# Optimization experiments

Hardware: AMD Instinct MI355X
Metric: run time of the kernel (lower is better)

## Reference

```python
import jax, jax.numpy as jnp
import numpy as np

B, SEQ, K, H = 4096, 50, 4, 64   # batch, seq_len, interest_num, hidden_size
ROUTING_TIMES = 3


def setup_inputs() -> dict:
    key = jax.random.key(0)
    k1, k2, k3 = jax.random.split(key, 3)
    mask = jax.random.randint(k1, (B, SEQ), 0, 2, dtype=jnp.int32)
    item_eb_hat = jax.random.normal(k2, (B, SEQ, K, H), dtype=jnp.float32)
    capsule_weight = jax.random.normal(k3, (B, K, SEQ), dtype=jnp.float32)
    return {"mask": mask, "item_eb_hat": item_eb_hat, "capsule_weight": capsule_weight}


def _squash(v):
    # v: [B, K, 1, H]
    cap_norm = jnp.sum(jnp.square(v), -1, keepdims=True)
    scalar = cap_norm / (1.0 + cap_norm) / jnp.sqrt(cap_norm + 1e-9)
    return scalar * v


def reference(mask, item_eb_hat, capsule_weight):
    # [B, seq, K, H] -> [B, K, seq, H]
    x = jnp.transpose(item_eb_hat.reshape(-1, SEQ, K, H), (0, 2, 1, 3))
    x_iter = jax.lax.stop_gradient(x)  # stop_grad=True in the module
    # attention mask broadcast to [B, K, seq]
    am = jnp.broadcast_to(mask[:, None, :], capsule_weight.shape)
    interest_capsule = None
    for i in range(ROUTING_TIMES):
        # torch F.softmax without dim on a 3D tensor -> dim=0 (batch axis); faithful.
        w = jax.nn.softmax(capsule_weight, axis=0)
        w = jnp.where(am == 0, jnp.zeros_like(w), w)[:, :, None, :]  # [B,K,1,seq]
        if i < ROUTING_TIMES - 1:
            interest_capsule = _squash(jnp.matmul(w, x_iter))          # [B,K,1,H]
            delta = jnp.matmul(x_iter, jnp.swapaxes(interest_capsule, -1, -2))  # [B,K,seq,1]
            capsule_weight = capsule_weight + delta.reshape(-1, K, SEQ)
        else:
            interest_capsule = _squash(jnp.matmul(w, x))               # [B,K,1,H]
    return interest_capsule.reshape(-1, K, H)
```

## Files before the change

### kernel.cpp

```cpp
#include <hip/hip_runtime.h>
#include <math.h>

#define BB 4096
#define SEQ 50
#define KK 4
#define HH 64
#define NCOL (KK*SEQ)

__global__ void colstats_kernel(const float* __restrict__ cw,
                                float* __restrict__ colmax,
                                float* __restrict__ colsum) {
    const int col = blockIdx.x;
    const int t = threadIdx.x;

    float m = -INFINITY, l = 0.f;
#pragma unroll
    for (int i = 0; i < BB / 256; i++) {
        float v = cw[(size_t)(i * 256 + t) * NCOL + col];
        float nm = fmaxf(m, v);
        l = l * __expf(m - nm) + __expf(v - nm);
        m = nm;
    }
#pragma unroll
    for (int off = 32; off >= 1; off >>= 1) {
        float om = __shfl_xor(m, off, 64);
        float ol = __shfl_xor(l, off, 64);
        float nm = fmaxf(m, om);
        l = l * __expf(m - nm) + ol * __expf(om - nm);
        m = nm;
    }
    __shared__ float sm[4], sl[4];
    const int wid = t >> 6;
    if ((t & 63) == 0) { sm[wid] = m; sl[wid] = l; }
    __syncthreads();
    if (t == 0) {
        m = sm[0]; l = sl[0];
#pragma unroll
        for (int w = 1; w < 4; w++) {
            float om = sm[w], ol = sl[w];
            float nm = fmaxf(m, om);
            l = l * __expf(m - nm) + ol * __expf(om - nm);
            m = nm;
        }
        colmax[col] = m;
        colsum[col] = l;
    }
}

template <bool FINAL>
__global__ void update_kernel(const float* __restrict__ cw_src,
                              float* __restrict__ cw_dst,
                              const float* __restrict__ x,
                              const int* __restrict__ mask,
                              const float* __restrict__ colmax,
                              const float* __restrict__ colsum,
                              float* __restrict__ out) {
    const int b = blockIdx.x;
    const int k = threadIdx.x >> 6;
    const int h = threadIdx.x & 63;

    const float* xp = x + (size_t)b * (SEQ * KK * HH) + k * HH + h;
    float xrow[SEQ];
#pragma unroll
    for (int s = 0; s < SEQ; s++) xrow[s] = xp[s * (KK * HH)];

    float wlane = 0.f, c = 0.f;
    if (h < SEQ) {
        const int col = k * SEQ + h;
        c = cw_src[(size_t)b * NCOL + col];
        float e = __expf(c - colmax[col]) / colsum[col];
        wlane = (mask[b * SEQ + h] != 0) ? e : 0.f;
    }

    float v = 0.f;
#pragma unroll
    for (int s = 0; s < SEQ; s++) {
        v = fmaf(__shfl(wlane, s, 64), xrow[s], v);
    }

    float n2 = v * v;
#pragma unroll
    for (int off = 32; off >= 1; off >>= 1) n2 += __shfl_xor(n2, off, 64);
    const float scalar = n2 / ((1.f + n2) * sqrtf(n2 + 1e-9f));
    v *= scalar;

    if (FINAL) {
        out[(size_t)b * (KK * HH) + k * HH + h] = v;
    } else {
        float myd = 0.f;
#pragma unroll
        for (int s = 0; s < SEQ; s++) {
            float p = xrow[s] * v;
#pragma unroll
            for (int off = 32; off >= 1; off >>= 1) p += __shfl_xor(p, off, 64);
            if (s == h) myd = p;
        }
        if (h < SEQ) {
            cw_dst[(size_t)b * NCOL + k * SEQ + h] = c + myd;
        }
    }
}

extern "C" void kernel_launch(void* const* d_in, const int* in_sizes, int n_in,
                              void* d_out, int out_size, void* d_ws, size_t ws_size,
                              hipStream_t stream) {
    const int*   mask  = (const int*)d_in[0];
    const float* x     = (const float*)d_in[1];
    const float* cw_in = (const float*)d_in[2];
    float* out = (float*)d_out;

    float* cw_ws  = (float*)d_ws;
    float* colmax = cw_ws + (size_t)BB * NCOL;
    float* colsum = colmax + NCOL;

    colstats_kernel<<<NCOL, 256, 0, stream>>>(cw_in, colmax, colsum);
    update_kernel<false><<<BB, 256, 0, stream>>>(cw_in, cw_ws, x, mask, colmax, colsum, nullptr);
    colstats_kernel<<<NCOL, 256, 0, stream>>>(cw_ws, colmax, colsum);
    update_kernel<false><<<BB, 256, 0, stream>>>(cw_ws, cw_ws, x, mask, colmax, colsum, nullptr);
    colstats_kernel<<<NCOL, 256, 0, stream>>>(cw_ws, colmax, colsum);
    update_kernel<true><<<BB, 256, 0, stream>>>(cw_ws, nullptr, x, mask, colmax, colsum, out);
}
```

Baseline: 419.1 us.

## Fuse column softmax statistics into update kernel via partial-sum atomics

Removes the separate column-statistics kernels. Each update pass now accumulates exp of the new capsule weights into 64 partition buffers with atomicAdd, and the next pass reduces those partitions into shared memory per block. The max subtraction is dropped, so the softmax is unstabilized and relies on the weights staying within exp range. Every block now redundantly sums 64x200 partials, and the atomics add contention.

```diff
diff --git a/kernel.cpp b/kernel.cpp
--- a/kernel.cpp
+++ b/kernel.cpp
@@ -6,77 +6,64 @@
 #define KK 4
 #define HH 64
 #define NCOL (KK*SEQ)
+#define NPART 64
+#define BPP (BB/NPART)
 
-__global__ void colstats_kernel(const float* __restrict__ cw,
-                                float* __restrict__ colmax,
-                                float* __restrict__ colsum) {
-    const int col = blockIdx.x;
+__global__ void init_kernel(const float* __restrict__ cw,
+                            float* __restrict__ part0,
+                            float* __restrict__ part1,
+                            float* __restrict__ part2) {
+    const int p = blockIdx.x;
     const int t = threadIdx.x;
-
-    float m = -INFINITY, l = 0.f;
-#pragma unroll
-    for (int i = 0; i < BB / 256; i++) {
-        float v = cw[(size_t)(i * 256 + t) * NCOL + col];
-        float nm = fmaxf(m, v);
-        l = l * __expf(m - nm) + __expf(v - nm);
-        m = nm;
-    }
-#pragma unroll
-    for (int off = 32; off >= 1; off >>= 1) {
-        float om = __shfl_xor(m, off, 64);
-        float ol = __shfl_xor(l, off, 64);
-        float nm = fmaxf(m, om);
-        l = l * __expf(m - nm) + ol * __expf(om - nm);
-        m = nm;
-    }
-    __shared__ float sm[4], sl[4];
-    const int wid = t >> 6;
-    if ((t & 63) == 0) { sm[wid] = m; sl[wid] = l; }
-    __syncthreads();
-    if (t == 0) {
-        m = sm[0]; l = sl[0];
-#pragma unroll
-        for (int w = 1; w < 4; w++) {
-            float om = sm[w], ol = sl[w];
-            float nm = fmaxf(m, om);
-            l = l * __expf(m - nm) + ol * __expf(om - nm);
-            m = nm;
-        }
-        colmax[col] = m;
-        colsum[col] = l;
+    if (t < NCOL) {
+        const float* row = cw + (size_t)p * BPP * NCOL + t;
+        float s = 0.f;
+#pragma unroll 8
+        for (int b = 0; b < BPP; b++) s += __expf(row[b * NCOL]);
+        part0[p * NCOL + t] = s;
+        part1[p * NCOL + t] = 0.f;
+        part2[p * NCOL + t] = 0.f;
     }
 }
 
-template <bool FINAL>
+template <int ITER>
 __global__ void update_kernel(const float* __restrict__ cw_src,
                               float* __restrict__ cw_dst,
                               const float* __restrict__ x,
                               const int* __restrict__ mask,
-                              const float* __restrict__ colmax,
-                              const float* __restrict__ colsum,
+                              const float* __restrict__ part_in,
+                              float* __restrict__ part_out,
                               float* __restrict__ out) {
     const int b = blockIdx.x;
     const int k = threadIdx.x >> 6;
     const int h = threadIdx.x & 63;
+
+    __shared__ float scol[NCOL];
+
+    if (threadIdx.x < NCOL) {
+        float s = 0.f;
+#pragma unroll 16
+        for (int p = 0; p < NPART; p++) s += part_in[p * NCOL + threadIdx.x];
+        scol[threadIdx.x] = s;
+    }
 
     const float* xp = x + (size_t)b * (SEQ * KK * HH) + k * HH + h;
     float xrow[SEQ];
 #pragma unroll
     for (int s = 0; s < SEQ; s++) xrow[s] = xp[s * (KK * HH)];
 
+    __syncthreads();
+
     float wlane = 0.f, c = 0.f;
     if (h < SEQ) {
-        const int col = k * SEQ + h;
-        c = cw_src[(size_t)b * NCOL + col];
-        float e = __expf(c - colmax[col]) / colsum[col];
+        c = cw_src[(size_t)b * NCOL + k * SEQ + h];
+        float e = __expf(c) / scol[k * SEQ + h];
         wlane = (mask[b * SEQ + h] != 0) ? e : 0.f;
     }
 
     float v = 0.f;
 #pragma unroll
-    for (int s = 0; s < SEQ; s++) {
-        v = fmaf(__shfl(wlane, s, 64), xrow[s], v);
-    }
+    for (int s = 0; s < SEQ; s++) v = fmaf(__shfl(wlane, s, 64), xrow[s], v);
 
     float n2 = v * v;
 #pragma unroll
@@ -84,7 +71,7 @@
     const float scalar = n2 / ((1.f + n2) * sqrtf(n2 + 1e-9f));
     v *= scalar;
 
-    if (FINAL) {
+    if (ITER == 2) {
         out[(size_t)b * (KK * HH) + k * HH + h] = v;
     } else {
         float myd = 0.f;
@@ -96,7 +83,9 @@
             if (s == h) myd = p;
         }
         if (h < SEQ) {
-            cw_dst[(size_t)b * NCOL + k * SEQ + h] = c + myd;
+            const float nc = c + myd;
+            cw_dst[(size_t)b * NCOL + k * SEQ + h] = nc;
+            atomicAdd(&part_out[(b >> 6) * NCOL + k * SEQ + h], __expf(nc));
         }
     }
 }
@@ -109,14 +98,13 @@
     const float* cw_in = (const float*)d_in[2];
     float* out = (float*)d_out;
 
-    float* cw_ws  = (float*)d_ws;
-    float* colmax = cw_ws + (size_t)BB * NCOL;
-    float* colsum = colmax + NCOL;
+    float* cw_ws = (float*)d_ws;
+    float* part0 = cw_ws + (size_t)BB * NCOL;
+    float* part1 = part0 + NPART * NCOL;
+    float* part2 = part1 + NPART * NCOL;
 
-    colstats_kernel<<<NCOL, 256, 0, stream>>>(cw_in, colmax, colsum);
-    update_kernel<false><<<BB, 256, 0, stream>>>(cw_in, cw_ws, x, mask, colmax, colsum, nullptr);
-    colstats_kernel<<<NCOL, 256, 0, stream>>>(cw_ws, colmax, colsum);
-    update_kernel<false><<<BB, 256, 0, stream>>>(cw_ws, cw_ws, x, mask, colmax, colsum, nullptr);
-    colstats_kernel<<<NCOL, 256, 0, stream>>>(cw_ws, colmax, colsum);
-    update_kernel<true><<<BB, 256, 0, stream>>>(cw_ws, nullptr, x, mask, colmax, colsum, out);
+    init_kernel<<<NPART, 256, 0, stream>>>(cw_in, part0, part1, part2);
+    update_kernel<0><<<BB, 256, 0, stream>>>(cw_in, cw_ws, x, mask, part0, part1, nullptr);
+    update_kernel<1><<<BB, 256, 0, stream>>>(cw_ws, cw_ws, x, mask, part1, part2, nullptr);
+    update_kernel<2><<<BB, 256, 0, stream>>>(cw_ws, nullptr, x, mask, part2, nullptr, out);
 }
```

New measurement: 401.5 us. 1.04x faster.
